# Kernel tuning notes

Measured on AMD Instinct MI355X. Metric: run time of the kernel, lower is better.

Reference implementation:

```python
import jax, jax.numpy as jnp
import numpy as np


def setup_inputs() -> dict:
    key = jax.random.key(0)
    ks = jax.random.split(key, 4)
    B, T, IN, H, OUT = 256, 128, 128, 256, 128
    s = 0.05  # small init scale to keep gates unsaturated
    return {
        "x": jax.random.normal(ks[0], (B, T, IN), dtype=jnp.float32),
        "hid_state": jnp.zeros((1, 3, B, H), dtype=jnp.float32),
        "Wx": jax.random.normal(ks[1], (IN, 3 * H), dtype=jnp.float32) * s,
        "bx": jnp.zeros((3 * H,), dtype=jnp.float32),
        "Wh": jax.random.normal(ks[2], (H, 3 * H), dtype=jnp.float32) * s,
        "bh": jnp.zeros((3 * H,), dtype=jnp.float32),
        "Wf": jax.random.normal(ks[3], (H, OUT), dtype=jnp.float32) * s,
        "bf": jnp.zeros((OUT,), dtype=jnp.float32),
    }


def reference(x, hid_state, Wx, bx, Wh, bh, Wf, bf):
    # x: (B, T, IN); hid_state: (num_layers=1, 3, B, H)
    h0 = hid_state[0]  # (3, B, H) three-component CRU hidden state

    def step(h, xt):
        gx = xt @ Wx + bx                      # (B, 3H)
        gh = h @ Wh + bh                       # (3, B, 3H)
        ir, iz, inn = jnp.split(gx, 3, axis=-1)
        hr, hz, hn = jnp.split(gh, 3, axis=-1)
        r = jax.nn.sigmoid(ir[None] + hr)      # (3, B, H)
        z = jax.nn.sigmoid(iz[None] + hz)
        n = jnp.tanh(inn[None] + r * hn)
        h_new = n + z * (h - n)                # GRU-style update, (3, B, H)
        return h_new, None

    hT, _ = jax.lax.scan(step, h0, jnp.swapaxes(x, 0, 1))  # scan over T
    feature = jnp.mean(hT, axis=1)                          # (3, H): mean over batch
    out = jnp.sum(hT, axis=0)                               # (B, H): sum over components
    out = jax.nn.elu(out @ Wf + bf)                         # (B, OUT)
    return out, feature
```

## Files before the change

kernel.cpp:

```cpp
#include <hip/hip_runtime.h>

#define B_   256
#define T_   128
#define IN_  128
#define H_   256
#define H3_  768
#define OUT_ 128

#define L2E  1.4426950408889634f

typedef unsigned short u16;
typedef u16   u16x4  __attribute__((ext_vector_type(4)));
typedef u16   u16x8  __attribute__((ext_vector_type(8)));
typedef __bf16 bf16x8 __attribute__((ext_vector_type(8)));
typedef float f32x4  __attribute__((ext_vector_type(4)));
typedef int   i32x4  __attribute__((ext_vector_type(4)));
typedef signed char c8x8 __attribute__((ext_vector_type(8)));

__device__ __forceinline__ float bf2f(u16 u) {
  unsigned int v = ((unsigned int)u) << 16;
  return __builtin_bit_cast(float, v);
}
__device__ __forceinline__ u16 f2bf(float f) {
  unsigned int u = __builtin_bit_cast(unsigned int, f);
  u += 0x7fffu + ((u >> 16) & 1u);
  return (u16)(u >> 16);
}
__device__ __forceinline__ f32x4 mfma16(bf16x8 a, bf16x8 b, f32x4 c) {
  return __builtin_amdgcn_mfma_f32_16x16x32_bf16(a, b, c, 0, 0, 0);
}
__device__ __forceinline__ i32x4 mfma8(i32x4 a, i32x4 b, i32x4 c) {
  return __builtin_amdgcn_mfma_i32_16x16x64_i8(a, b, c, 0, 0, 0);
}
__device__ __forceinline__ float exp2f_(float x) {
#if __has_builtin(__builtin_amdgcn_exp2f)
  return __builtin_amdgcn_exp2f(x);
#else
  return __builtin_exp2f(x);
#endif
}
__device__ __forceinline__ float rcp_(float x) { return __builtin_amdgcn_rcpf(x); }

__device__ __forceinline__ int pick4i(i32x4 v, int e) {
  int r = v[0];
  r = (e == 1) ? v[1] : r;
  r = (e == 2) ? v[2] : r;
  r = (e == 3) ? v[3] : r;
  return r;
}

__global__ __launch_bounds__(1024) void prep0(const float* __restrict__ Wx,
                                              const float* __restrict__ Wh,
                                              u16* __restrict__ WxT,
                                              float* __restrict__ sw) {
  const int bid = blockIdx.x;
  if (bid < 96) {
    int o = bid * 1024 + threadIdx.x;
    int n = o >> 7, k = o & 127;
    WxT[o] = f2bf(Wx[(size_t)k * H3_ + n]);
  } else {
    __shared__ float red[16][64];
    const int n0 = (bid - 96) * 64;
    const int nl = threadIdx.x & 63, kg = threadIdx.x >> 6;
    float m = 1e-30f;
    #pragma unroll
    for (int i = 0; i < 16; ++i)
      m = fmaxf(m, fabsf(Wh[(size_t)(kg * 16 + i) * H3_ + n0 + nl]));
    red[kg][nl] = m;
    __syncthreads();
    if (threadIdx.x < 64) {
      float v = m;
      #pragma unroll
      for (int i = 1; i < 16; ++i) v = fmaxf(v, red[i][nl]);
      sw[n0 + nl] = v * (1.f / 127.f);
    }
  }
}

__global__ __launch_bounds__(512) void prep1(const float* __restrict__ x,
                                             const u16* __restrict__ WxT,
                                             const float* __restrict__ bx,
                                             const float* __restrict__ bh,
                                             const float* __restrict__ Wh,
                                             const float* __restrict__ sw,
                                             u16* __restrict__ gxw,
                                             signed char* __restrict__ whp8) {
  __shared__ __align__(16) char smem[(128 * 136 + 384 * 136) * 2];
  const int bid = blockIdx.x;
  const int tid = threadIdx.x;

  if (bid < 48) {
    int o8 = bid * 512 + tid;
    int tp  = o8 / 48;
    int idx = o8 % 48;
    int g  = idx >> 4;
    int s  = (idx >> 3) & 1;
    int kk = (idx >> 1) & 3;
    int j8 = idx & 1;
    int l  = tp & 63, w = tp >> 6;
    int n  = g * 256 + w * 32 + s * 16 + (l & 15);
    int kbase = kk * 64 + ((l >> 4) & 3) * 16 + j8 * 8;
    float rs = rcp_(sw[n]);
    c8x8 v;
    #pragma unroll
    for (int j = 0; j < 8; ++j) {
      float q = __builtin_rintf(Wh[(size_t)(kbase + j) * H3_ + n] * rs);
      v[j] = (signed char)(int)q;
    }
    *(c8x8*)(whp8 + (size_t)o8 * 8) = v;
    return;
  }

  u16 (*As)[136] = (u16(*)[136])smem;
  u16 (*Bs)[136] = (u16(*)[136])(smem + 128 * 136 * 2);
  u16 (*St)[392] = (u16(*)[392])smem;

  const int gb = bid - 48;
  const int mt = gb & 255;
  const int n0 = (gb >> 8) * 384;
  const int m0 = mt * 128;
  const int t  = mt >> 1;
  const int brow0 = (mt & 1) * 128;
  const int w = tid >> 6, lane = tid & 63, quad = lane >> 4, r = lane & 15;
  const int wm = w >> 2, wn = w & 3;

  {
    int row = tid >> 2;
    int colc = (tid & 3) * 4;
    const float* s = x + ((size_t)(brow0 + row) * T_ + t) * IN_ + colc;
    #pragma unroll
    for (int c4 = 0; c4 < 8; ++c4) {
      f32x4 v = *(const f32x4*)(s + c4 * 16);
      u16x4 b;
      b[0] = f2bf(v[0]); b[1] = f2bf(v[1]); b[2] = f2bf(v[2]); b[3] = f2bf(v[3]);
      *(u16x4*)&As[row][colc + c4 * 16] = b;
    }
  }
  {
    #pragma unroll
    for (int i = 0; i < 12; ++i) {
      int idx = tid + i * 512;
      int row = idx >> 4, col8 = (idx & 15) * 8;
      *(u16x8*)&Bs[row][col8] = *(const u16x8*)(WxT + (size_t)(n0 + row) * IN_ + col8);
    }
  }
  __syncthreads();

  f32x4 acc[4][6];
  #pragma unroll
  for (int i = 0; i < 4; ++i)
    #pragma unroll
    for (int j = 0; j < 6; ++j)
      acc[i][j] = (f32x4){0.f, 0.f, 0.f, 0.f};

  #pragma unroll
  for (int kk = 0; kk < 4; ++kk) {
    bf16x8 a[4];
    #pragma unroll
    for (int m2 = 0; m2 < 4; ++m2)
      a[m2] = *(const bf16x8*)&As[wm * 64 + m2 * 16 + r][kk * 32 + quad * 8];
    #pragma unroll
    for (int n2 = 0; n2 < 6; ++n2) {
      bf16x8 b = *(const bf16x8*)&Bs[wn * 96 + n2 * 16 + r][kk * 32 + quad * 8];
      #pragma unroll
      for (int m2 = 0; m2 < 4; ++m2)
        acc[m2][n2] = mfma16(a[m2], b, acc[m2][n2]);
    }
  }

  __syncthreads();

  #pragma unroll
  for (int m2 = 0; m2 < 4; ++m2)
    #pragma unroll
    for (int n2 = 0; n2 < 6; ++n2) {
      int nl = wn * 96 + n2 * 16 + r;
      int n  = n0 + nl;
      float sc = (n < 512) ? L2E : (2.f * L2E);
      float bias = bx[n] + (n < 512 ? bh[n] : 0.f);
      #pragma unroll
      for (int e = 0; e < 4; ++e) {
        int mrow = wm * 64 + m2 * 16 + quad * 4 + e;
        St[mrow][nl] = f2bf((acc[m2][n2][e] + bias) * sc);
      }
    }
  __syncthreads();

  #pragma unroll
  for (int i = 0; i < 12; ++i) {
    int idx = tid + i * 512;
    int row = idx / 48, c8 = (idx % 48) * 8;
    *(u16x8*)(gxw + (size_t)(m0 + row) * H3_ + n0 + c8) = *(const u16x8*)&St[row][c8];
  }
}

__global__ __launch_bounds__(512)
void cru_scan(const float* __restrict__ hid,
              const signed char* __restrict__ whp8,
              const float* __restrict__ sw,
              const float* __restrict__ bh,
              const u16*  __restrict__ gx,
              float* __restrict__ hT) {
  __shared__ __align__(16) signed char h8[2][4][288];

  const int bid = blockIdx.x;
  const int c   = bid >> 6;
  const int b0  = (bid & 63) << 2;
  const int tid = threadIdx.x;
  const int lane = tid & 63, quad = lane >> 4, m = lane & 15;
  const int w  = tid >> 6;
  const int bb = m & 3;
  const int e  = m >> 2;
  const int hcol0 = w * 32 + quad * 4 + e;
  const int hcol1 = hcol0 + 16;

  i32x4 bfr[3][2][4];
  {
    const signed char* wp = whp8 + (size_t)tid * 384;
    #pragma unroll
    for (int g = 0; g < 3; ++g)
      #pragma unroll
      for (int s = 0; s < 2; ++s)
        #pragma unroll
        for (int kk = 0; kk < 4; ++kk)
          bfr[g][s][kk] = *(const i32x4*)(wp + g * 128 + s * 64 + kk * 16);
  }

  const float dqR0 = sw[hcol0]       * (L2E / 127.f);
  const float dqR1 = sw[hcol1]       * (L2E / 127.f);
  const float dqZ0 = sw[256 + hcol0] * (L2E / 127.f);
  const float dqZ1 = sw[256 + hcol1] * (L2E / 127.f);
  const float dqN0 = sw[512 + hcol0] * (2.f * L2E / 127.f);
  const float dqN1 = sw[512 + hcol1] * (2.f * L2E / 127.f);

  const size_t hrow0 = (size_t)(c * 256 + b0 + bb) * 256 + hcol0;
  float hx0 = hid[hrow0];
  float hx1 = hid[hrow0 + 16];
  h8[0][bb][hcol0] = (signed char)(int)__builtin_rintf(fminf(fmaxf(hx0, -1.f), 1.f) * 127.f);
  h8[0][bb][hcol1] = (signed char)(int)__builtin_rintf(fminf(fmaxf(hx1, -1.f), 1.f) * 127.f);
  const float bn0 = bh[512 + hcol0] * (2.f * L2E);
  const float bn1 = bh[512 + hcol1] * (2.f * L2E);

  const u16* gxp = gx + (size_t)(b0 + bb) * H3_ + hcol0;
  const int rbase = bb * 288 + quad * 16;

  u16 xr0 = gxp[0],   xr1 = gxp[16];
  u16 xz0 = gxp[256], xz1 = gxp[272];
  u16 xn0 = gxp[512], xn1 = gxp[528];
  const u16* gxs = gxp + (size_t)(B_ * H3_);

  __syncthreads();

  #pragma unroll 2
  for (int t = 0; t < T_; ++t) {
    const int sel = t & 1;

    const signed char* hb = &h8[sel][0][0];
    i32x4 f0 = *(const i32x4*)(hb + rbase);
    i32x4 f1 = *(const i32x4*)(hb + rbase + 64);
    i32x4 f2 = *(const i32x4*)(hb + rbase + 128);
    i32x4 f3 = *(const i32x4*)(hb + rbase + 192);

    __builtin_amdgcn_s_setprio(1);
    i32x4 aR0 = {0,0,0,0}, aR1 = {0,0,0,0};
    i32x4 aZ0 = {0,0,0,0}, aZ1 = {0,0,0,0};
    i32x4 aN0 = {0,0,0,0}, aN1 = {0,0,0,0};
#define STEP_(kk, fk) \
    aR0 = mfma8(bfr[0][0][kk], fk, aR0); \
    aR1 = mfma8(bfr[0][1][kk], fk, aR1); \
    aZ0 = mfma8(bfr[1][0][kk], fk, aZ0); \
    aZ1 = mfma8(bfr[1][1][kk], fk, aZ1); \
    aN0 = mfma8(bfr[2][0][kk], fk, aN0); \
    aN1 = mfma8(bfr[2][1][kk], fk, aN1);
    STEP_(0, f0)
    STEP_(1, f1)
    STEP_(2, f2)
    STEP_(3, f3)
#undef STEP_
    __builtin_amdgcn_s_setprio(0);

    u16 nr0 = gxs[0],   nr1 = gxs[16];
    u16 nz0 = gxs[256], nz1 = gxs[272];
    u16 nn0_ = gxs[512], nn1_ = gxs[528];
    gxs += B_ * H3_;

    {
      float gR = (float)pick4i(aR0, e) * dqR0;
      float gZ = (float)pick4i(aZ0, e) * dqZ0;
      float sr = rcp_(1.f + exp2f_(-(bf2f(xr0) + gR)));
      float sz = rcp_(1.f + exp2f_(-(bf2f(xz0) + gZ)));
      float gN = (float)pick4i(aN0, e) * dqN0;
      float nv = bf2f(xn0) + sr * (gN + bn0);
      float nn = fmaf(2.f, rcp_(1.f + exp2f_(-nv)), -1.f);
      float hv = nn + sz * (hx0 - nn);
      hx0 = hv;
      h8[sel ^ 1][bb][hcol0] = (signed char)(int)__builtin_rintf(hv * 127.f);
    }
    {
      float gR = (float)pick4i(aR1, e) * dqR1;
      float gZ = (float)pick4i(aZ1, e) * dqZ1;
      float sr = rcp_(1.f + exp2f_(-(bf2f(xr1) + gR)));
      float sz = rcp_(1.f + exp2f_(-(bf2f(xz1) + gZ)));
      float gN = (float)pick4i(aN1, e) * dqN1;
      float nv = bf2f(xn1) + sr * (gN + bn1);
      float nn = fmaf(2.f, rcp_(1.f + exp2f_(-nv)), -1.f);
      float hv = nn + sz * (hx1 - nn);
      hx1 = hv;
      h8[sel ^ 1][bb][hcol1] = (signed char)(int)__builtin_rintf(hv * 127.f);
    }
    xr0 = nr0; xr1 = nr1; xz0 = nz0; xz1 = nz1; xn0 = nn0_; xn1 = nn1_;
    __syncthreads();
  }

  hT[hrow0] = hx0;
  hT[hrow0 + 16] = hx1;
}

__global__ __launch_bounds__(128) void finalize(const float* __restrict__ hT,
                                                const float* __restrict__ Wf,
                                                const float* __restrict__ bfv,
                                                float* __restrict__ out) {
  __shared__ float hsum[256];
  const int bid = blockIdx.x, tid = threadIdx.x;
  if (bid < 256) {
    const int b = bid;
    for (int k = tid; k < 256; k += 128)
      hsum[k] = hT[((size_t)(0 * 256 + b)) * 256 + k]
              + hT[((size_t)(1 * 256 + b)) * 256 + k]
              + hT[((size_t)(2 * 256 + b)) * 256 + k];
    __syncthreads();
    float acc = bfv[tid];
    #pragma unroll 8
    for (int k = 0; k < 256; ++k)
      acc = fmaf(hsum[k], Wf[(size_t)k * OUT_ + tid], acc);
    float rv = acc > 0.f ? acc : (__expf(acc) - 1.f);
    out[b * OUT_ + tid] = rv;
  } else {
    const int idx = bid - 256;
    const int c = idx >> 1, j = ((idx & 1) << 7) + tid;
    float sum = 0.f;
    #pragma unroll 4
    for (int b = 0; b < 256; ++b)
      sum += hT[((size_t)(c * 256 + b)) * 256 + j];
    out[B_ * OUT_ + c * 256 + j] = sum * (1.f / 256.f);
  }
}

extern "C" void kernel_launch(void* const* d_in, const int* in_sizes, int n_in,
                              void* d_out, int out_size, void* d_ws, size_t ws_size,
                              hipStream_t stream) {
  const float* x   = (const float*)d_in[0];
  const float* hid = (const float*)d_in[1];
  const float* Wx  = (const float*)d_in[2];
  const float* bx  = (const float*)d_in[3];
  const float* Wh  = (const float*)d_in[4];
  const float* bh  = (const float*)d_in[5];
  const float* Wf  = (const float*)d_in[6];
  const float* bf_ = (const float*)d_in[7];
  float* out = (float*)d_out;

  char* ws = (char*)d_ws;
  u16* WxT   = (u16*)ws;
  u16* gxw   = (u16*)(ws + (1 << 18));
  size_t off = (1 << 18) + (size_t)T_ * B_ * H3_ * 2;
  float* hTw = (float*)(ws + off);
  off += (size_t)3 * 256 * 256 * 4;
  signed char* whp8 = (signed char*)(ws + off);
  off += (size_t)512 * 384;
  float* sww = (float*)(ws + off);

  prep0<<<108, 1024, 0, stream>>>(Wx, Wh, WxT, sww);
  prep1<<<560, 512, 0, stream>>>(x, WxT, bx, bh, Wh, sww, gxw, whp8);
  cru_scan<<<192, 512, 0, stream>>>(hid, whp8, sww, bh, gxw, hTw);
  finalize<<<262, 128, 0, stream>>>(hTw, Wf, bf_, out);
}
```

Measured before the change: 204.6 us.

## Add 1024-thread scan variant selected by register count of 512 version

Adds a cru_scan1024 kernel where each thread owns one hidden column instead of two, halving per-thread weight registers and doubling wavefronts per block to increase latency hiding in the serial recurrence. The original kernel gets launch_bounds(512,1), and the host inspects its register count once to choose which variant runs. The 1024-thread path launches when the 512 version uses fewer than 140 registers. The extra waves add cost to the per-step barrier.

```diff
diff --git a/kernel.cpp b/kernel.cpp
--- a/kernel.cpp
+++ b/kernel.cpp
@@ -194,13 +194,13 @@
   }
 }
 
-__global__ __launch_bounds__(512)
-void cru_scan(const float* __restrict__ hid,
-              const signed char* __restrict__ whp8,
-              const float* __restrict__ sw,
-              const float* __restrict__ bh,
-              const u16*  __restrict__ gx,
-              float* __restrict__ hT) {
+__global__ __launch_bounds__(512, 1)
+void cru_scan512(const float* __restrict__ hid,
+                 const signed char* __restrict__ whp8,
+                 const float* __restrict__ sw,
+                 const float* __restrict__ bh,
+                 const u16*  __restrict__ gx,
+                 float* __restrict__ hT) {
   __shared__ __align__(16) signed char h8[2][4][288];
 
   const int bid = blockIdx.x;
@@ -314,6 +314,103 @@
 
   hT[hrow0] = hx0;
   hT[hrow0 + 16] = hx1;
+}
+
+__global__ __launch_bounds__(1024)
+void cru_scan1024(const float* __restrict__ hid,
+                  const signed char* __restrict__ whp8,
+                  const float* __restrict__ sw,
+                  const float* __restrict__ bh,
+                  const u16*  __restrict__ gx,
+                  float* __restrict__ hT) {
+  __shared__ __align__(16) signed char h8[2][4][288];
+
+  const int bid = blockIdx.x;
+  const int c   = bid >> 6;
+  const int b0  = (bid & 63) << 2;
+  const int tid = threadIdx.x;
+  const int lane = tid & 63, quad = lane >> 4, m = lane & 15;
+  const int w  = tid >> 6;
+  const int bb = m & 3;
+  const int e  = m >> 2;
+  const int hcol = w * 16 + quad * 4 + e;
+
+  i32x4 bfr[3][4];
+  {
+    const signed char* wp = whp8
+        + (size_t)(((tid >> 7) << 6) | (tid & 63)) * 384
+        + (size_t)((tid >> 6) & 1) * 64;
+    #pragma unroll
+    for (int g = 0; g < 3; ++g)
+      #pragma unroll
+      for (int kk = 0; kk < 4; ++kk)
+        bfr[g][kk] = *(const i32x4*)(wp + g * 128 + kk * 16);
+  }
+
+  const float dqR = sw[hcol]       * (L2E / 127.f);
+  const float dqZ = sw[256 + hcol] * (L2E / 127.f);
+  const float dqN = sw[512 + hcol] * (2.f * L2E / 127.f);
+
+  const size_t hrow = (size_t)(c * 256 + b0 + bb) * 256 + hcol;
+  float hx = hid[hrow];
+  h8[0][bb][hcol] = (signed char)(int)__builtin_rintf(fminf(fmaxf(hx, -1.f), 1.f) * 127.f);
+  const float bn0 = bh[512 + hcol] * (2.f * L2E);
+
+  const u16* gxp = gx + (size_t)(b0 + bb) * H3_ + hcol;
+  const int rbase = bb * 288 + quad * 16;
+
+  u16 xr = gxp[0], xz = gxp[256], xn = gxp[512];
+  const u16* gxs = gxp + (size_t)(B_ * H3_);
+
+  __syncthreads();
+
+  #pragma unroll 2
+  for (int t = 0; t < T_; ++t) {
+    const int sel = t & 1;
+
+    const signed char* hb = &h8[sel][0][0];
+    i32x4 f0 = *(const i32x4*)(hb + rbase);
+    i32x4 f1 = *(const i32x4*)(hb + rbase + 64);
+    i32x4 f2 = *(const i32x4*)(hb + rbase + 128);
+    i32x4 f3 = *(const i32x4*)(hb + rbase + 192);
+
+    __builtin_amdgcn_s_setprio(1);
+    i32x4 accR = {0, 0, 0, 0};
+    i32x4 accZ = {0, 0, 0, 0};
+    i32x4 accN = {0, 0, 0, 0};
+    accR = mfma8(bfr[0][0], f0, accR);
+    accZ = mfma8(bfr[1][0], f0, accZ);
+    accN = mfma8(bfr[2][0], f0, accN);
+    accR = mfma8(bfr[0][1], f1, accR);
+    accZ = mfma8(bfr[1][1], f1, accZ);
+    accN = mfma8(bfr[2][1], f1, accN);
+    accR = mfma8(bfr[0][2], f2, accR);
+    accZ = mfma8(bfr[1][2], f2, accZ);
+    accN = mfma8(bfr[2][2], f2, accN);
+    accR = mfma8(bfr[0][3], f3, accR);
+    accZ = mfma8(bfr[1][3], f3, accZ);
+    accN = mfma8(bfr[2][3], f3, accN);
+    __builtin_amdgcn_s_setprio(0);
+
+    u16 nxr = gxs[0], nxz = gxs[256], nxn = gxs[512];
+    gxs += B_ * H3_;
+
+    float gR = (float)pick4i(accR, e) * dqR;
+    float gZ = (float)pick4i(accZ, e) * dqZ;
+    float sr = rcp_(1.f + exp2f_(-(bf2f(xr) + gR)));
+    float sz = rcp_(1.f + exp2f_(-(bf2f(xz) + gZ)));
+
+    float gN = (float)pick4i(accN, e) * dqN;
+    float nv = bf2f(xn) + sr * (gN + bn0);
+    float nn = fmaf(2.f, rcp_(1.f + exp2f_(-nv)), -1.f);
+    float hv = nn + sz * (hx - nn);
+    hx = hv;
+    h8[sel ^ 1][bb][hcol] = (signed char)(int)__builtin_rintf(hv * 127.f);
+    xr = nxr; xz = nxz; xn = nxn;
+    __syncthreads();
+  }
+
+  hT[hrow] = hx;
 }
 
 __global__ __launch_bounds__(128) void finalize(const float* __restrict__ hT,
@@ -369,8 +466,20 @@
   off += (size_t)512 * 384;
   float* sww = (float*)(ws + off);
 
+  static int scan_variant = -1;
+  if (scan_variant < 0) {
+    hipFuncAttributes attr;
+    scan_variant = 0;
+    if (hipFuncGetAttributes(&attr, (const void*)cru_scan512) == hipSuccess &&
+        attr.numRegs >= 140)
+      scan_variant = 1;
+  }
+
   prep0<<<108, 1024, 0, stream>>>(Wx, Wh, WxT, sww);
   prep1<<<560, 512, 0, stream>>>(x, WxT, bx, bh, Wh, sww, gxw, whp8);
-  cru_scan<<<192, 512, 0, stream>>>(hid, whp8, sww, bh, gxw, hTw);
+  if (scan_variant == 1)
+    cru_scan512<<<192, 512, 0, stream>>>(hid, whp8, sww, bh, gxw, hTw);
+  else
+    cru_scan1024<<<192, 1024, 0, stream>>>(hid, whp8, sww, bh, gxw, hTw);
   finalize<<<262, 128, 0, stream>>>(hTw, Wf, bf_, out);
 }
```

After: 205.0 us. No clear change (+0.2%).
